# Performance work log

Measured on AMD Instinct MI355X. Metric: run time of the kernel, lower is better.

## Reference

```python
import jax, jax.numpy as jnp
import numpy as np

B, C, H, W, D = 2, 96, 64, 64, 32
NUM_HEADS = 8

def setup_inputs() -> dict:
    key = jax.random.key(0)
    kx, kq, kk, kv, kp = jax.random.split(key, 5)
    x = jax.random.normal(kx, (B, C, H, W, D), dtype=jnp.float32)
    # torch nn.Linear weights: [out_features, in_features]; 1x1x1 conv proj as [C_out, C_in]
    s = 0.02
    Wq = jax.random.normal(kq, (C, C), dtype=jnp.float32) * s
    Wk = jax.random.normal(kk, (C, C), dtype=jnp.float32) * s
    Wv = jax.random.normal(kv, (C, C), dtype=jnp.float32) * s
    Wproj = jax.random.normal(kp, (C, C), dtype=jnp.float32) * s
    return {"x": x, "Wq": Wq, "Wk": Wk, "Wv": Wv, "Wproj": Wproj}

def reference(x, Wq, Wk, Wv, Wproj):
    b, c, h, w, d = x.shape
    n = h * w * d
    nh = NUM_HEADS
    hd = c // nh  # head dim (qk_dim == v_dim == dim here)
    # [B, C, H, W, D] -> [B, N, C]
    xf = jnp.transpose(x.reshape(b, c, n), (0, 2, 1))
    def to_heads(W):
        y = jnp.einsum('bnc,oc->bno', xf, W)  # nn.Linear: x @ W^T
        return jnp.transpose(y.reshape(b, n, nh, hd), (0, 2, 1, 3))  # [B, H, N, hd]
    q = to_heads(Wq)
    k = to_heads(Wk)
    v = to_heads(Wv)
    q = jax.nn.softmax(q, axis=-1)   # over head dim
    k = jax.nn.softmax(k, axis=-2)   # over tokens N
    # linear attention: contract over N first -> tiny [B, H, hd, hd] context
    context = jnp.einsum('bhnd,bhne->bhde', k, v)
    attn = jnp.einsum('bhnd,bhde->bhne', q, context)  # [B, H, N, hd]
    out = jnp.transpose(attn, (0, 2, 1, 3)).reshape(b, n, c)  # [B, N, C]
    out = jnp.transpose(out, (0, 2, 1)).reshape(b, c, h, w, d)
    # 1x1x1 conv projection (bias=False) == channel mixing
    out = jnp.einsum('oc,bchwd->bohwd', Wproj, out)
    return out
```

## Files before the change

kernel.cpp:

```cpp
#include <hip/hip_runtime.h>


typedef _Float16 half_t;
typedef _Float16 half8 __attribute__((ext_vector_type(8)));
typedef float f32x4 __attribute__((ext_vector_type(4)));

#define MFMA16 __builtin_amdgcn_mfma_f32_16x16x32_f16
#define NSH 17
#define NP 16

__device__ __forceinline__ int swz(int row, int colh) {
  return (row * 256 + colh * 2) ^ ((row & 7) << 4);
}

__global__ void wcvt(const float* __restrict__ Wq, const float* __restrict__ Wk,
                     const float* __restrict__ Wv, half_t* __restrict__ WqH,
                     half_t* __restrict__ WkH, half_t* __restrict__ WvH) {
  const int g = blockIdx.x * 256 + threadIdx.x;
  WqH[g] = (half_t)Wq[g];
  WkH[g] = (half_t)Wk[g];
  WvH[g] = (half_t)Wv[g];
}

__global__ __launch_bounds__(256, 3)
void p1(const float* __restrict__ x, const half_t* __restrict__ Wk,
        const half_t* __restrict__ Wv, float* __restrict__ part) {
  __shared__ __align__(16) char smem[49152];

  const int tid  = threadIdx.x;
  const int lane = tid & 63, l15 = lane & 15, quad = lane >> 4, wid = tid >> 6;
  const int b  = blockIdx.x >> 10;
  const int n0 = (blockIdx.x & 1023) << 7;

  float xv[48];
  {
    const float* xb = x + (((size_t)(b * 96 + quad * 8)) << NSH) + n0 + wid * 32 + l15;
#pragma unroll
    for (int ks = 0; ks < 3; ++ks)
#pragma unroll
      for (int j = 0; j < 8; ++j)
#pragma unroll
        for (int ct = 0; ct < 2; ++ct)
          xv[(ks * 8 + j) * 2 + ct] = xb[(((size_t)(ks * 32 + j)) << NSH) + ct * 16];
  }
  half8 bf[3][2];
#pragma unroll
  for (int ks = 0; ks < 3; ++ks)
#pragma unroll
    for (int ct = 0; ct < 2; ++ct)
#pragma unroll
      for (int j = 0; j < 8; ++j)
        bf[ks][ct][j] = (half_t)xv[(ks * 8 + j) * 2 + ct];

  f32x4 acc[6][2];
#pragma unroll
  for (int rt = 0; rt < 6; ++rt)
#pragma unroll
    for (int ct = 0; ct < 2; ++ct) acc[rt][ct] = (f32x4){0.f, 0.f, 0.f, 0.f};
#pragma unroll
  for (int ks = 0; ks < 3; ++ks) {
    half8 af[6];
#pragma unroll
    for (int rt = 0; rt < 6; ++rt)
      af[rt] = *(const half8*)&Wk[(rt * 16 + l15) * 96 + ks * 32 + quad * 8];
#pragma unroll
    for (int rt = 0; rt < 6; ++rt)
#pragma unroll
      for (int ct = 0; ct < 2; ++ct)
        acc[rt][ct] = MFMA16(af[rt], bf[ks][ct], acc[rt][ct], 0, 0, 0);
  }
#pragma unroll
  for (int rt = 0; rt < 6; ++rt)
#pragma unroll
    for (int ct = 0; ct < 2; ++ct)
#pragma unroll
      for (int i = 0; i < 4; ++i) {
        int row = rt * 16 + quad * 4 + i;
        int col = (wid * 2 + ct) * 16 + l15;
        *(half_t*)(smem + swz(row, col)) = (half_t)__expf(acc[rt][ct][i]);
      }

#pragma unroll
  for (int rt = 0; rt < 6; ++rt)
#pragma unroll
    for (int ct = 0; ct < 2; ++ct) acc[rt][ct] = (f32x4){0.f, 0.f, 0.f, 0.f};
#pragma unroll
  for (int ks = 0; ks < 3; ++ks) {
    half8 af[6];
#pragma unroll
    for (int rt = 0; rt < 6; ++rt)
      af[rt] = *(const half8*)&Wv[(rt * 16 + l15) * 96 + ks * 32 + quad * 8];
#pragma unroll
    for (int rt = 0; rt < 6; ++rt)
#pragma unroll
      for (int ct = 0; ct < 2; ++ct)
        acc[rt][ct] = MFMA16(af[rt], bf[ks][ct], acc[rt][ct], 0, 0, 0);
  }
#pragma unroll
  for (int rt = 0; rt < 6; ++rt)
#pragma unroll
    for (int ct = 0; ct < 2; ++ct)
#pragma unroll
      for (int i = 0; i < 4; ++i) {
        int row = rt * 16 + quad * 4 + i;
        int col = (wid * 2 + ct) * 16 + l15;
        *(half_t*)(smem + 24576 + swz(row, col)) = (half_t)acc[rt][ct][i];
      }
  __syncthreads();

  float* dst = part + (size_t)((blockIdx.x & (NP - 1)) * 2 + b) * 1248;
#pragma unroll
  for (int hh = 0; hh < 2; ++hh) {
    const int h = wid * 2 + hh;
    int row = h * 12 + l15; row = row > 95 ? 95 : row;
    f32x4 c = (f32x4){0.f, 0.f, 0.f, 0.f};
#pragma unroll
    for (int ks = 0; ks < 4; ++ks) {
      const int off = swz(row, ks * 32 + quad * 8);
      half8 a  = *(const half8*)(smem + off);
      half8 bv = *(const half8*)(smem + 24576 + off);
      c = MFMA16(a, bv, c, 0, 0, 0);
    }
#pragma unroll
    for (int i = 0; i < 4; ++i) {
      int d = quad * 4 + i, e = l15;
      if (d < 12 && e < 12) atomicAdd(&dst[h * 144 + d * 12 + e], c[i]);
    }
  }
  if (tid < 96) {
    float s = 0.f;
#pragma unroll
    for (int j = 0; j < 16; ++j) {
      half8 v = *(const half8*)(smem + swz(tid, j * 8));
#pragma unroll
      for (int e = 0; e < 8; ++e) s += (float)v[e];
    }
    atomicAdd(&dst[1152 + tid], s);
  }
}

__global__ void kB(const float* __restrict__ part, const float* __restrict__ Wproj,
                   half_t* __restrict__ Mt) {
  const int g = blockIdx.x * 256 + threadIdx.x;
  const int b = g / (96 * 96);
  const int rem = g % (96 * 96);
  const int o = rem / 96;
  const int r = rem % 96;
  const int h = r / 12, d = r % 12;
  float s = 0.f;
#pragma unroll
  for (int p = 0; p < NP; ++p) s += part[(size_t)(p * 2 + b) * 1248 + 1152 + r];
  float acc = 0.f;
#pragma unroll
  for (int e = 0; e < 12; ++e) {
    float ce = 0.f;
#pragma unroll
    for (int p = 0; p < NP; ++p)
      ce += part[(size_t)(p * 2 + b) * 1248 + h * 144 + d * 12 + e];
    acc = fmaf(ce, Wproj[o * 96 + h * 12 + e], acc);
  }
  Mt[(size_t)(b * 96 + o) * 96 + r] = (half_t)(acc / s);
}

__global__ __launch_bounds__(256, 4)
void p3(const float* __restrict__ x, const half_t* __restrict__ Wq,
        const half_t* __restrict__ Mt, float* __restrict__ out) {
  __shared__ __align__(16) char smem[32768];

  const int tid  = threadIdx.x;
  const int lane = tid & 63, l15 = lane & 15, quad = lane >> 4, wid = tid >> 6;
  const int b  = blockIdx.x >> 10;
  const int n0 = (blockIdx.x & 1023) << 7;

  float xv[48];
  {
    const float* xb = x + (((size_t)(b * 96 + quad * 8)) << NSH) + n0 + wid * 32 + l15;
#pragma unroll
    for (int ks = 0; ks < 3; ++ks)
#pragma unroll
      for (int j = 0; j < 8; ++j)
#pragma unroll
        for (int ct = 0; ct < 2; ++ct)
          xv[(ks * 8 + j) * 2 + ct] = xb[(((size_t)(ks * 32 + j)) << NSH) + ct * 16];
  }
  half8 bf[3][2];
#pragma unroll
  for (int ks = 0; ks < 3; ++ks)
#pragma unroll
    for (int ct = 0; ct < 2; ++ct)
#pragma unroll
      for (int j = 0; j < 8; ++j)
        bf[ks][ct][j] = (half_t)xv[(ks * 8 + j) * 2 + ct];

  f32x4 acc[6][2];
#pragma unroll
  for (int rt = 0; rt < 6; ++rt)
#pragma unroll
    for (int ct = 0; ct < 2; ++ct) acc[rt][ct] = (f32x4){0.f, 0.f, 0.f, 0.f};
#pragma unroll
  for (int ks = 0; ks < 3; ++ks) {
    half8 af[6];
#pragma unroll
    for (int rt = 0; rt < 6; ++rt)
      af[rt] = *(const half8*)&Wq[(rt * 16 + l15) * 96 + ks * 32 + quad * 8];
#pragma unroll
    for (int rt = 0; rt < 6; ++rt)
#pragma unroll
      for (int ct = 0; ct < 2; ++ct)
        acc[rt][ct] = MFMA16(af[rt], bf[ks][ct], acc[rt][ct], 0, 0, 0);
  }
#pragma unroll
  for (int rt = 0; rt < 6; ++rt)
#pragma unroll
    for (int ct = 0; ct < 2; ++ct)
#pragma unroll
      for (int i = 0; i < 4; ++i) {
        int row = rt * 16 + quad * 4 + i;
        int col = (wid * 2 + ct) * 16 + l15;
        *(half_t*)(smem + swz(col, row)) = (half_t)acc[rt][ct][i];
      }
  __syncthreads();

  {
    const int n = tid & 127, hg = tid >> 7;
    float q[48];
#pragma unroll
    for (int j = 0; j < 6; ++j) {
      half8 v = *(const half8*)(smem + swz(n, hg * 48 + j * 8));
#pragma unroll
      for (int e = 0; e < 8; ++e) q[j * 8 + e] = (float)v[e];
    }
#pragma unroll
    for (int hh = 0; hh < 4; ++hh) {
      float* ql = q + hh * 12;
      float m = ql[0];
#pragma unroll
      for (int j = 1; j < 12; ++j) m = fmaxf(m, ql[j]);
      float s = 0.f;
#pragma unroll
      for (int j = 0; j < 12; ++j) { ql[j] = __expf(ql[j] - m); s += ql[j]; }
      const float inv = 1.0f / s;
#pragma unroll
      for (int j = 0; j < 12; ++j) ql[j] *= inv;
    }
#pragma unroll
    for (int j = 0; j < 6; ++j) {
      half8 w;
#pragma unroll
      for (int e = 0; e < 8; ++e) w[e] = (half_t)q[j * 8 + e];
      *(half8*)(smem + swz(n, hg * 48 + j * 8)) = w;
    }
  }
  __syncthreads();

#pragma unroll
  for (int rt = 0; rt < 6; ++rt)
#pragma unroll
    for (int ct = 0; ct < 2; ++ct) acc[rt][ct] = (f32x4){0.f, 0.f, 0.f, 0.f};
#pragma unroll
  for (int ks = 0; ks < 3; ++ks) {
    half8 af[6], bq[2];
#pragma unroll
    for (int rt = 0; rt < 6; ++rt)
      af[rt] = *(const half8*)&Mt[(size_t)b * 9216 + (rt * 16 + l15) * 96 + ks * 32 + quad * 8];
#pragma unroll
    for (int ct = 0; ct < 2; ++ct)
      bq[ct] = *(const half8*)(smem + swz((wid * 2 + ct) * 16 + l15, ks * 32 + quad * 8));
#pragma unroll
    for (int rt = 0; rt < 6; ++rt)
#pragma unroll
      for (int ct = 0; ct < 2; ++ct)
        acc[rt][ct] = MFMA16(af[rt], bq[ct], acc[rt][ct], 0, 0, 0);
  }
#pragma unroll
  for (int rt = 0; rt < 6; ++rt)
#pragma unroll
    for (int ct = 0; ct < 2; ++ct)
#pragma unroll
      for (int i = 0; i < 4; ++i) {
        int row = rt * 16 + quad * 4 + i;
        int col = (wid * 2 + ct) * 16 + l15;
        out[(((size_t)(b * 96 + row)) << NSH) + n0 + col] = acc[rt][ct][i];
      }
}

extern "C" void kernel_launch(void* const* d_in, const int* in_sizes, int n_in,
                              void* d_out, int out_size, void* d_ws, size_t ws_size,
                              hipStream_t stream) {
  const float* x     = (const float*)d_in[0];
  const float* Wq    = (const float*)d_in[1];
  const float* Wk    = (const float*)d_in[2];
  const float* Wv    = (const float*)d_in[3];
  const float* Wproj = (const float*)d_in[4];
  float* out = (float*)d_out;
  float* ws  = (float*)d_ws;

  float*  part = ws;
  half_t* Mt   = (half_t*)(ws + NP * 2 * 1248);
  half_t* WqH  = (half_t*)(ws + NP * 2 * 1248 + 9216);
  half_t* WkH  = WqH + 9216;
  half_t* WvH  = WkH + 9216;

  hipMemsetAsync(part, 0, NP * 2 * 1248 * sizeof(float), stream);
  wcvt<<<36, 256, 0, stream>>>(Wq, Wk, Wv, WqH, WkH, WvH);
  p1<<<2048, 256, 0, stream>>>(x, WkH, WvH, part);
  kB<<<72, 256, 0, stream>>>(part, Wproj, Mt);
  p3<<<2048, 256, 0, stream>>>(x, WqH, Mt, out);
}
```

Measured before the change: 246.3 us.

## Use persistent 4-tile blocks with register prefetch and fold context reduction into output kernel

Each block of the K/V-context and output kernels now processes four 128-token tiles, preloading the next tile's x values into registers while computing the current one. The memset is folded into the weight-conversion kernel, and the kB kernel is removed: each output block reduces the partial contexts and builds the projected context matrix in LDS. This cuts launch count and per-block setup. In exchange every output block redundantly recomputes the 96x96 matrix, and occupancy is lower because of larger LDS use and launch bounds of 2.

```diff
diff --git a/kernel.cpp b/kernel.cpp
--- a/kernel.cpp
+++ b/kernel.cpp
@@ -13,28 +13,32 @@
   return (row * 256 + colh * 2) ^ ((row & 7) << 4);
 }
 
-__global__ void wcvt(const float* __restrict__ Wq, const float* __restrict__ Wk,
-                     const float* __restrict__ Wv, half_t* __restrict__ WqH,
-                     half_t* __restrict__ WkH, half_t* __restrict__ WvH) {
+__global__ void k1(const float* __restrict__ Wq, const float* __restrict__ Wk,
+                   const float* __restrict__ Wv, half_t* __restrict__ WqH,
+                   half_t* __restrict__ WkH, half_t* __restrict__ WvH,
+                   float* __restrict__ part) {
   const int g = blockIdx.x * 256 + threadIdx.x;
   WqH[g] = (half_t)Wq[g];
   WkH[g] = (half_t)Wk[g];
   WvH[g] = (half_t)Wv[g];
-}
-
-__global__ __launch_bounds__(256, 3)
-void p1(const float* __restrict__ x, const half_t* __restrict__ Wk,
-        const half_t* __restrict__ Wv, float* __restrict__ part) {
+  for (int i = g; i < NP * 2 * 1248; i += 9216) part[i] = 0.f;
+}
+
+__global__ __launch_bounds__(256, 2)
+void pA(const float* __restrict__ x, const half_t* __restrict__ WkH,
+        const half_t* __restrict__ WvH, float* __restrict__ part) {
   __shared__ __align__(16) char smem[49152];
 
   const int tid  = threadIdx.x;
   const int lane = tid & 63, l15 = lane & 15, quad = lane >> 4, wid = tid >> 6;
-  const int b  = blockIdx.x >> 10;
-  const int n0 = (blockIdx.x & 1023) << 7;
+  const int bid  = blockIdx.x;
+  const int b    = bid >> 8;
+  const float* xbase = x + (((size_t)(b * 96 + quad * 8)) << NSH) + wid * 32 + l15;
+  float* dst = part + (size_t)((bid & (NP - 1)) * 2 + b) * 1248;
 
   float xv[48];
   {
-    const float* xb = x + (((size_t)(b * 96 + quad * 8)) << NSH) + n0 + wid * 32 + l15;
+    const float* xb = xbase + (((bid & 255) * 4 + 0) << 7);
 #pragma unroll
     for (int ks = 0; ks < 3; ++ks)
 #pragma unroll
@@ -43,138 +47,135 @@
         for (int ct = 0; ct < 2; ++ct)
           xv[(ks * 8 + j) * 2 + ct] = xb[(((size_t)(ks * 32 + j)) << NSH) + ct * 16];
   }
-  half8 bf[3][2];
-#pragma unroll
-  for (int ks = 0; ks < 3; ++ks)
-#pragma unroll
-    for (int ct = 0; ct < 2; ++ct)
-#pragma unroll
-      for (int j = 0; j < 8; ++j)
-        bf[ks][ct][j] = (half_t)xv[(ks * 8 + j) * 2 + ct];
-
-  f32x4 acc[6][2];
-#pragma unroll
-  for (int rt = 0; rt < 6; ++rt)
-#pragma unroll
-    for (int ct = 0; ct < 2; ++ct) acc[rt][ct] = (f32x4){0.f, 0.f, 0.f, 0.f};
-#pragma unroll
-  for (int ks = 0; ks < 3; ++ks) {
-    half8 af[6];
-#pragma unroll
-    for (int rt = 0; rt < 6; ++rt)
-      af[rt] = *(const half8*)&Wk[(rt * 16 + l15) * 96 + ks * 32 + quad * 8];
-#pragma unroll
-    for (int rt = 0; rt < 6; ++rt)
-#pragma unroll
-      for (int ct = 0; ct < 2; ++ct)
-        acc[rt][ct] = MFMA16(af[rt], bf[ks][ct], acc[rt][ct], 0, 0, 0);
-  }
-#pragma unroll
-  for (int rt = 0; rt < 6; ++rt)
-#pragma unroll
-    for (int ct = 0; ct < 2; ++ct)
+
+#pragma unroll
+  for (int tt = 0; tt < 4; ++tt) {
+    half8 bf[3][2];
+#pragma unroll
+    for (int ks = 0; ks < 3; ++ks)
+#pragma unroll
+      for (int ct = 0; ct < 2; ++ct)
+#pragma unroll
+        for (int j = 0; j < 8; ++j)
+          bf[ks][ct][j] = (half_t)xv[(ks * 8 + j) * 2 + ct];
+
+    if (tt < 3) {
+      const float* xb = xbase + (((bid & 255) * 4 + tt + 1) << 7);
+#pragma unroll
+      for (int ks = 0; ks < 3; ++ks)
+#pragma unroll
+        for (int j = 0; j < 8; ++j)
+#pragma unroll
+          for (int ct = 0; ct < 2; ++ct)
+            xv[(ks * 8 + j) * 2 + ct] = xb[(((size_t)(ks * 32 + j)) << NSH) + ct * 16];
+    }
+
+    f32x4 acc[6][2];
+#pragma unroll
+    for (int rt = 0; rt < 6; ++rt)
+#pragma unroll
+      for (int ct = 0; ct < 2; ++ct) acc[rt][ct] = (f32x4){0.f, 0.f, 0.f, 0.f};
+#pragma unroll
+    for (int ks = 0; ks < 3; ++ks) {
+      half8 af[6];
+#pragma unroll
+      for (int rt = 0; rt < 6; ++rt)
+        af[rt] = *(const half8*)&WkH[(rt * 16 + l15) * 96 + ks * 32 + quad * 8];
+#pragma unroll
+      for (int rt = 0; rt < 6; ++rt)
+#pragma unroll
+        for (int ct = 0; ct < 2; ++ct)
+          acc[rt][ct] = MFMA16(af[rt], bf[ks][ct], acc[rt][ct], 0, 0, 0);
+    }
+#pragma unroll
+    for (int rt = 0; rt < 6; ++rt)
+#pragma unroll
+      for (int ct = 0; ct < 2; ++ct)
+#pragma unroll
+        for (int i = 0; i < 4; ++i) {
+          int row = rt * 16 + quad * 4 + i;
+          int col = (wid * 2 + ct) * 16 + l15;
+          *(half_t*)(smem + swz(row, col)) = (half_t)__expf(acc[rt][ct][i]);
+        }
+
+#pragma unroll
+    for (int rt = 0; rt < 6; ++rt)
+#pragma unroll
+      for (int ct = 0; ct < 2; ++ct) acc[rt][ct] = (f32x4){0.f, 0.f, 0.f, 0.f};
+#pragma unroll
+    for (int ks = 0; ks < 3; ++ks) {
+      half8 af[6];
+#pragma unroll
+      for (int rt = 0; rt < 6; ++rt)
+        af[rt] = *(const half8*)&WvH[(rt * 16 + l15) * 96 + ks * 32 + quad * 8];
+#pragma unroll
+      for (int rt = 0; rt < 6; ++rt)
+#pragma unroll
+        for (int ct = 0; ct < 2; ++ct)
+          acc[rt][ct] = MFMA16(af[rt], bf[ks][ct], acc[rt][ct], 0, 0, 0);
+    }
+#pragma unroll
+    for (int rt = 0; rt < 6; ++rt)
+#pragma unroll
+      for (int ct = 0; ct < 2; ++ct)
+#pragma unroll
+        for (int i = 0; i < 4; ++i) {
+          int row = rt * 16 + quad * 4 + i;
+          int col = (wid * 2 + ct) * 16 + l15;
+          *(half_t*)(smem + 24576 + swz(row, col)) = (half_t)acc[rt][ct][i];
+        }
+    __syncthreads();
+
+#pragma unroll
+    for (int hh = 0; hh < 2; ++hh) {
+      const int h = wid * 2 + hh;
+      int row = h * 12 + l15; row = row > 95 ? 95 : row;
+      f32x4 c = (f32x4){0.f, 0.f, 0.f, 0.f};
+#pragma unroll
+      for (int ks = 0; ks < 4; ++ks) {
+        const int off = swz(row, ks * 32 + quad * 8);
+        half8 a  = *(const half8*)(smem + off);
+        half8 bv = *(const half8*)(smem + 24576 + off);
+        c = MFMA16(a, bv, c, 0, 0, 0);
+      }
 #pragma unroll
       for (int i = 0; i < 4; ++i) {
-        int row = rt * 16 + quad * 4 + i;
-        int col = (wid * 2 + ct) * 16 + l15;
-        *(half_t*)(smem + swz(row, col)) = (half_t)__expf(acc[rt][ct][i]);
-      }
-
-#pragma unroll
-  for (int rt = 0; rt < 6; ++rt)
-#pragma unroll
-    for (int ct = 0; ct < 2; ++ct) acc[rt][ct] = (f32x4){0.f, 0.f, 0.f, 0.f};
-#pragma unroll
-  for (int ks = 0; ks < 3; ++ks) {
-    half8 af[6];
-#pragma unroll
-    for (int rt = 0; rt < 6; ++rt)
-      af[rt] = *(const half8*)&Wv[(rt * 16 + l15) * 96 + ks * 32 + quad * 8];
-#pragma unroll
-    for (int rt = 0; rt < 6; ++rt)
-#pragma unroll
-      for (int ct = 0; ct < 2; ++ct)
-        acc[rt][ct] = MFMA16(af[rt], bf[ks][ct], acc[rt][ct], 0, 0, 0);
-  }
-#pragma unroll
-  for (int rt = 0; rt < 6; ++rt)
-#pragma unroll
-    for (int ct = 0; ct < 2; ++ct)
-#pragma unroll
-      for (int i = 0; i < 4; ++i) {
-        int row = rt * 16 + quad * 4 + i;
-        int col = (wid * 2 + ct) * 16 + l15;
-        *(half_t*)(smem + 24576 + swz(row, col)) = (half_t)acc[rt][ct][i];
-      }
-  __syncthreads();
-
-  float* dst = part + (size_t)((blockIdx.x & (NP - 1)) * 2 + b) * 1248;
-#pragma unroll
-  for (int hh = 0; hh < 2; ++hh) {
-    const int h = wid * 2 + hh;
-    int row = h * 12 + l15; row = row > 95 ? 95 : row;
-    f32x4 c = (f32x4){0.f, 0.f, 0.f, 0.f};
-#pragma unroll
-    for (int ks = 0; ks < 4; ++ks) {
-      const int off = swz(row, ks * 32 + quad * 8);
-      half8 a  = *(const half8*)(smem + off);
-      half8 bv = *(const half8*)(smem + 24576 + off);
-      c = MFMA16(a, bv, c, 0, 0, 0);
-    }
-#pragma unroll
-    for (int i = 0; i < 4; ++i) {
-      int d = quad * 4 + i, e = l15;
-      if (d < 12 && e < 12) atomicAdd(&dst[h * 144 + d * 12 + e], c[i]);
-    }
-  }
-  if (tid < 96) {
-    float s = 0.f;
-#pragma unroll
-    for (int j = 0; j < 16; ++j) {
-      half8 v = *(const half8*)(smem + swz(tid, j * 8));
-#pragma unroll
-      for (int e = 0; e < 8; ++e) s += (float)v[e];
-    }
-    atomicAdd(&dst[1152 + tid], s);
-  }
-}
-
-__global__ void kB(const float* __restrict__ part, const float* __restrict__ Wproj,
-                   half_t* __restrict__ Mt) {
-  const int g = blockIdx.x * 256 + threadIdx.x;
-  const int b = g / (96 * 96);
-  const int rem = g % (96 * 96);
-  const int o = rem / 96;
-  const int r = rem % 96;
-  const int h = r / 12, d = r % 12;
-  float s = 0.f;
-#pragma unroll
-  for (int p = 0; p < NP; ++p) s += part[(size_t)(p * 2 + b) * 1248 + 1152 + r];
-  float acc = 0.f;
-#pragma unroll
-  for (int e = 0; e < 12; ++e) {
-    float ce = 0.f;
-#pragma unroll
-    for (int p = 0; p < NP; ++p)
-      ce += part[(size_t)(p * 2 + b) * 1248 + h * 144 + d * 12 + e];
-    acc = fmaf(ce, Wproj[o * 96 + h * 12 + e], acc);
-  }
-  Mt[(size_t)(b * 96 + o) * 96 + r] = (half_t)(acc / s);
-}
-
-__global__ __launch_bounds__(256, 4)
-void p3(const float* __restrict__ x, const half_t* __restrict__ Wq,
-        const half_t* __restrict__ Mt, float* __restrict__ out) {
-  __shared__ __align__(16) char smem[32768];
+        int d = quad * 4 + i, e = l15;
+        if (d < 12 && e < 12) atomicAdd(&dst[h * 144 + d * 12 + e], c[i]);
+      }
+    }
+    if (tid < 96) {
+      float s = 0.f;
+#pragma unroll
+      for (int j = 0; j < 16; ++j) {
+        half8 v = *(const half8*)(smem + swz(tid, j * 8));
+#pragma unroll
+        for (int e = 0; e < 8; ++e) s += (float)v[e];
+      }
+      atomicAdd(&dst[1152 + tid], s);
+    }
+    __syncthreads();
+  }
+}
+
+__global__ __launch_bounds__(256, 2)
+void pC(const float* __restrict__ x, const half_t* __restrict__ WqH,
+        const float* __restrict__ Wproj, const float* __restrict__ part,
+        float* __restrict__ out) {
+  __shared__ __align__(16) char smem[53248];
+  half_t* Mt_lds = (half_t*)smem;
+  float*  ctxS   = (float*)(smem + 20480);
+  char*   qs     = smem + 20480;
 
   const int tid  = threadIdx.x;
   const int lane = tid & 63, l15 = lane & 15, quad = lane >> 4, wid = tid >> 6;
-  const int b  = blockIdx.x >> 10;
-  const int n0 = (blockIdx.x & 1023) << 7;
+  const int bid  = blockIdx.x;
+  const int b    = bid >> 8;
+  const float* xbase = x + (((size_t)(b * 96 + quad * 8)) << NSH) + wid * 32 + l15;
 
   float xv[48];
   {
-    const float* xb = x + (((size_t)(b * 96 + quad * 8)) << NSH) + n0 + wid * 32 + l15;
+    const float* xb = xbase + (((bid & 255) * 4 + 0) << 7);
 #pragma unroll
     for (int ks = 0; ks < 3; ++ks)
 #pragma unroll
@@ -183,105 +184,143 @@
         for (int ct = 0; ct < 2; ++ct)
           xv[(ks * 8 + j) * 2 + ct] = xb[(((size_t)(ks * 32 + j)) << NSH) + ct * 16];
   }
-  half8 bf[3][2];
-#pragma unroll
-  for (int ks = 0; ks < 3; ++ks)
-#pragma unroll
-    for (int ct = 0; ct < 2; ++ct)
-#pragma unroll
-      for (int j = 0; j < 8; ++j)
-        bf[ks][ct][j] = (half_t)xv[(ks * 8 + j) * 2 + ct];
-
-  f32x4 acc[6][2];
-#pragma unroll
-  for (int rt = 0; rt < 6; ++rt)
-#pragma unroll
-    for (int ct = 0; ct < 2; ++ct) acc[rt][ct] = (f32x4){0.f, 0.f, 0.f, 0.f};
-#pragma unroll
-  for (int ks = 0; ks < 3; ++ks) {
-    half8 af[6];
-#pragma unroll
-    for (int rt = 0; rt < 6; ++rt)
-      af[rt] = *(const half8*)&Wq[(rt * 16 + l15) * 96 + ks * 32 + quad * 8];
-#pragma unroll
-    for (int rt = 0; rt < 6; ++rt)
-#pragma unroll
-      for (int ct = 0; ct < 2; ++ct)
-        acc[rt][ct] = MFMA16(af[rt], bf[ks][ct], acc[rt][ct], 0, 0, 0);
-  }
-#pragma unroll
-  for (int rt = 0; rt < 6; ++rt)
-#pragma unroll
-    for (int ct = 0; ct < 2; ++ct)
-#pragma unroll
-      for (int i = 0; i < 4; ++i) {
-        int row = rt * 16 + quad * 4 + i;
-        int col = (wid * 2 + ct) * 16 + l15;
-        *(half_t*)(smem + swz(col, row)) = (half_t)acc[rt][ct][i];
-      }
+
+  for (int idx = tid; idx < 1248; idx += 256) {
+    float s = 0.f;
+#pragma unroll
+    for (int p = 0; p < NP; ++p) s += part[(size_t)(p * 2 + b) * 1248 + idx];
+    ctxS[idx] = s;
+  }
   __syncthreads();
-
-  {
-    const int n = tid & 127, hg = tid >> 7;
-    float q[48];
-#pragma unroll
-    for (int j = 0; j < 6; ++j) {
-      half8 v = *(const half8*)(smem + swz(n, hg * 48 + j * 8));
-#pragma unroll
-      for (int e = 0; e < 8; ++e) q[j * 8 + e] = (float)v[e];
-    }
-#pragma unroll
-    for (int hh = 0; hh < 4; ++hh) {
-      float* ql = q + hh * 12;
-      float m = ql[0];
-#pragma unroll
-      for (int j = 1; j < 12; ++j) m = fmaxf(m, ql[j]);
-      float s = 0.f;
-#pragma unroll
-      for (int j = 0; j < 12; ++j) { ql[j] = __expf(ql[j] - m); s += ql[j]; }
-      const float inv = 1.0f / s;
-#pragma unroll
-      for (int j = 0; j < 12; ++j) ql[j] *= inv;
-    }
-#pragma unroll
-    for (int j = 0; j < 6; ++j) {
-      half8 w;
-#pragma unroll
-      for (int e = 0; e < 8; ++e) w[e] = (half_t)q[j * 8 + e];
-      *(half8*)(smem + swz(n, hg * 48 + j * 8)) = w;
-    }
+#pragma unroll
+  for (int i = 0; i < 36; ++i) {
+    int g = i * 256 + tid;
+    int o = g / 96, r = g - o * 96;
+    int h = r / 12, d = r - h * 12;
+    float s = ctxS[1152 + r];
+    float acc = 0.f;
+#pragma unroll
+    for (int e = 0; e < 12; ++e)
+      acc = fmaf(ctxS[h * 144 + d * 12 + e], Wproj[o * 96 + h * 12 + e], acc);
+    Mt_lds[o * 104 + r] = (half_t)(acc / s);
   }
   __syncthreads();
 
 #pragma unroll
-  for (int rt = 0; rt < 6; ++rt)
-#pragma unroll
-    for (int ct = 0; ct < 2; ++ct) acc[rt][ct] = (f32x4){0.f, 0.f, 0.f, 0.f};
-#pragma unroll
-  for (int ks = 0; ks < 3; ++ks) {
-    half8 af[6], bq[2];
-#pragma unroll
-    for (int rt = 0; rt < 6; ++rt)
-      af[rt] = *(const half8*)&Mt[(size_t)b * 9216 + (rt * 16 + l15) * 96 + ks * 32 + quad * 8];
-#pragma unroll
-    for (int ct = 0; ct < 2; ++ct)
-      bq[ct] = *(const half8*)(smem + swz((wid * 2 + ct) * 16 + l15, ks * 32 + quad * 8));
-#pragma unroll
-    for (int rt = 0; rt < 6; ++rt)
-#pragma unroll
-      for (int ct = 0; ct < 2; ++ct)
-        acc[rt][ct] = MFMA16(af[rt], bq[ct], acc[rt][ct], 0, 0, 0);
-  }
-#pragma unroll
-  for (int rt = 0; rt < 6; ++rt)
-#pragma unroll
-    for (int ct = 0; ct < 2; ++ct)
-#pragma unroll
-      for (int i = 0; i < 4; ++i) {
-        int row = rt * 16 + quad * 4 + i;
-        int col = (wid * 2 + ct) * 16 + l15;
-        out[(((size_t)(b * 96 + row)) << NSH) + n0 + col] = acc[rt][ct][i];
-      }
+  for (int tt = 0; tt < 4; ++tt) {
+    half8 bf[3][2];
+#pragma unroll
+    for (int ks = 0; ks < 3; ++ks)
+#pragma unroll
+      for (int ct = 0; ct < 2; ++ct)
+#pragma unroll
+        for (int j = 0; j < 8; ++j)
+          bf[ks][ct][j] = (half_t)xv[(ks * 8 + j) * 2 + ct];
+
+    if (tt < 3) {
+      const float* xb = xbase + (((bid & 255) * 4 + tt + 1) << 7);
+#pragma unroll
+      for (int ks = 0; ks < 3; ++ks)
+#pragma unroll
+        for (int j = 0; j < 8; ++j)
+#pragma unroll
+          for (int ct = 0; ct < 2; ++ct)
+            xv[(ks * 8 + j) * 2 + ct] = xb[(((size_t)(ks * 32 + j)) << NSH) + ct * 16];
+    }
+
+    const int n0 = (((bid & 255) * 4 + tt)) << 7;
+    f32x4 acc[6][2];
+#pragma unroll
+    for (int rt = 0; rt < 6; ++rt)
+#pragma unroll
+      for (int ct = 0; ct < 2; ++ct) acc[rt][ct] = (f32x4){0.f, 0.f, 0.f, 0.f};
+#pragma unroll
+    for (int ks = 0; ks < 3; ++ks) {
+      half8 af[6];
+#pragma unroll
+      for (int rt = 0; rt < 6; ++rt)
+        af[rt] = *(const half8*)&WqH[(rt * 16 + l15) * 96 + ks * 32 + quad * 8];
+#pragma unroll
+      for (int rt = 0; rt < 6; ++rt)
+#pragma unroll
+        for (int ct = 0; ct < 2; ++ct)
+          acc[rt][ct] = MFMA16(af[rt], bf[ks][ct], acc[rt][ct], 0, 0, 0);
+    }
+#pragma unroll
+    for (int rt = 0; rt < 6; ++rt)
+#pragma unroll
+      for (int ct = 0; ct < 2; ++ct)
+#pragma unroll
+        for (int i = 0; i < 4; ++i) {
+          int row = rt * 16 + quad * 4 + i;
+          int col = (wid * 2 + ct) * 16 + l15;
+          *(half_t*)(qs + swz(col, row)) = (half_t)acc[rt][ct][i];
+        }
+    __syncthreads();
+
+    {
+      const int n = tid & 127, hg = tid >> 7;
+      float q[48];
+#pragma unroll
+      for (int j = 0; j < 6; ++j) {
+        half8 v = *(const half8*)(qs + swz(n, hg * 48 + j * 8));
+#pragma unroll
+        for (int e = 0; e < 8; ++e) q[j * 8 + e] = (float)v[e];
+      }
+#pragma unroll
+      for (int hh = 0; hh < 4; ++hh) {
+        float* ql = q + hh * 12;
+        float m = ql[0];
+#pragma unroll
+        for (int j = 1; j < 12; ++j) m = fmaxf(m, ql[j]);
+        float s = 0.f;
+#pragma unroll
+        for (int j = 0; j < 12; ++j) { ql[j] = __expf(ql[j] - m); s += ql[j]; }
+        const float inv = 1.0f / s;
+#pragma unroll
+        for (int j = 0; j < 12; ++j) ql[j] *= inv;
+      }
+#pragma unroll
+      for (int j = 0; j < 6; ++j) {
+        half8 w;
+#pragma unroll
+        for (int e = 0; e < 8; ++e) w[e] = (half_t)q[j * 8 + e];
+        *(half8*)(qs + swz(n, hg * 48 + j * 8)) = w;
+      }
+    }
+    __syncthreads();
+
+#pragma unroll
+    for (int rt = 0; rt < 6; ++rt)
+#pragma unroll
+      for (int ct = 0; ct < 2; ++ct) acc[rt][ct] = (f32x4){0.f, 0.f, 0.f, 0.f};
+#pragma unroll
+    for (int ks = 0; ks < 3; ++ks) {
+      half8 af[6], bq[2];
+#pragma unroll
+      for (int rt = 0; rt < 6; ++rt)
+        af[rt] = *(const half8*)(smem + (rt * 16 + l15) * 208 + (ks * 32 + quad * 8) * 2);
+#pragma unroll
+      for (int ct = 0; ct < 2; ++ct)
+        bq[ct] = *(const half8*)(qs + swz((wid * 2 + ct) * 16 + l15, ks * 32 + quad * 8));
+#pragma unroll
+      for (int rt = 0; rt < 6; ++rt)
+#pragma unroll
+        for (int ct = 0; ct < 2; ++ct)
+          acc[rt][ct] = MFMA16(af[rt], bq[ct], acc[rt][ct], 0, 0, 0);
+    }
+#pragma unroll
+    for (int rt = 0; rt < 6; ++rt)
+#pragma unroll
+      for (int ct = 0; ct < 2; ++ct)
+#pragma unroll
+        for (int i = 0; i < 4; ++i) {
+          int row = rt * 16 + quad * 4 + i;
+          int col = (wid * 2 + ct) * 16 + l15;
+          out[(((size_t)(b * 96 + row)) << NSH) + n0 + col] = acc[rt][ct][i];
+        }
+    __syncthreads();
+  }
 }
 
 extern "C" void kernel_launch(void* const* d_in, const int* in_sizes, int n_in,
@@ -296,14 +335,11 @@
   float* ws  = (float*)d_ws;
 
   float*  part = ws;
-  half_t* Mt   = (half_t*)(ws + NP * 2 * 1248);
-  half_t* WqH  = (half_t*)(ws + NP * 2 * 1248 + 9216);
+  half_t* WqH  = (half_t*)(ws + NP * 2 * 1248);
   half_t* WkH  = WqH + 9216;
   half_t* WvH  = WkH + 9216;
 
-  hipMemsetAsync(part, 0, NP * 2 * 1248 * sizeof(float), stream);
-  wcvt<<<36, 256, 0, stream>>>(Wq, Wk, Wv, WqH, WkH, WvH);
-  p1<<<2048, 256, 0, stream>>>(x, WkH, WvH, part);
-  kB<<<72, 256, 0, stream>>>(part, Wproj, Mt);
-  p3<<<2048, 256, 0, stream>>>(x, WqH, Mt, out);
-}
+  k1<<<36, 256, 0, stream>>>(Wq, Wk, Wv, WqH, WkH, WvH, part);
+  pA<<<512, 256, 0, stream>>>(x, WkH, WvH, part);
+  pC<<<512, 256, 0, stream>>>(x, WqH, Wproj, part, out);
+}
```

After: 271.3 us. 10.2% more time.

## Halve per-block token tile, double partial slots, fold memset into weight kernel

Applied to the files above, without the earlier changes.

Both main kernels now process 64 tokens per block instead of 128, which doubles the grid to 4096 blocks, halves shared memory and registers per block, and raises p1's occupancy bound from 3 to 4. The partial-sum buffer grows from 16 to 32 slots to spread atomic contention over more blocks. The separate memset is folded into the weight-conversion kernel, removing one launch. In exchange, each block reuses its weight fragments over fewer tokens, and twice as many blocks issue atomics.

```diff
diff --git a/kernel.cpp b/kernel.cpp
--- a/kernel.cpp
+++ b/kernel.cpp
@@ -7,118 +7,108 @@
 
 #define MFMA16 __builtin_amdgcn_mfma_f32_16x16x32_f16
 #define NSH 17
-#define NP 16
-
-__device__ __forceinline__ int swz(int row, int colh) {
+#define NP 32
+
+__device__ __forceinline__ int swz64(int row, int colh) {
+  return (row * 128 + colh * 2) ^ ((row & 7) << 4);
+}
+__device__ __forceinline__ int swz128(int row, int colh) {
   return (row * 256 + colh * 2) ^ ((row & 7) << 4);
 }
 
-__global__ void wcvt(const float* __restrict__ Wq, const float* __restrict__ Wk,
-                     const float* __restrict__ Wv, half_t* __restrict__ WqH,
-                     half_t* __restrict__ WkH, half_t* __restrict__ WvH) {
+__global__ void k1(const float* __restrict__ Wq, const float* __restrict__ Wk,
+                   const float* __restrict__ Wv, half_t* __restrict__ WqH,
+                   half_t* __restrict__ WkH, half_t* __restrict__ WvH,
+                   float* __restrict__ part) {
   const int g = blockIdx.x * 256 + threadIdx.x;
   WqH[g] = (half_t)Wq[g];
   WkH[g] = (half_t)Wk[g];
   WvH[g] = (half_t)Wv[g];
-}
-
-__global__ __launch_bounds__(256, 3)
-void p1(const float* __restrict__ x, const half_t* __restrict__ Wk,
-        const half_t* __restrict__ Wv, float* __restrict__ part) {
-  __shared__ __align__(16) char smem[49152];
+  for (int i = g; i < NP * 2 * 1248; i += 9216) part[i] = 0.f;
+}
+
+__global__ __launch_bounds__(256, 4)
+void pA(const float* __restrict__ x, const half_t* __restrict__ WkH,
+        const half_t* __restrict__ WvH, float* __restrict__ part) {
+  __shared__ __align__(16) char smem[24576];
 
   const int tid  = threadIdx.x;
   const int lane = tid & 63, l15 = lane & 15, quad = lane >> 4, wid = tid >> 6;
-  const int b  = blockIdx.x >> 10;
-  const int n0 = (blockIdx.x & 1023) << 7;
-
-  float xv[48];
+  const int bid  = blockIdx.x;
+  const int b    = bid >> 11;
+  const int n0   = (bid & 2047) << 6;
+  float* dst = part + (size_t)((bid & (NP - 1)) * 2 + b) * 1248;
+
+  half8 bf[3];
   {
-    const float* xb = x + (((size_t)(b * 96 + quad * 8)) << NSH) + n0 + wid * 32 + l15;
-#pragma unroll
-    for (int ks = 0; ks < 3; ++ks)
-#pragma unroll
-      for (int j = 0; j < 8; ++j)
-#pragma unroll
-        for (int ct = 0; ct < 2; ++ct)
-          xv[(ks * 8 + j) * 2 + ct] = xb[(((size_t)(ks * 32 + j)) << NSH) + ct * 16];
-  }
-  half8 bf[3][2];
-#pragma unroll
-  for (int ks = 0; ks < 3; ++ks)
-#pragma unroll
-    for (int ct = 0; ct < 2; ++ct)
-#pragma unroll
-      for (int j = 0; j < 8; ++j)
-        bf[ks][ct][j] = (half_t)xv[(ks * 8 + j) * 2 + ct];
-
-  f32x4 acc[6][2];
-#pragma unroll
-  for (int rt = 0; rt < 6; ++rt)
-#pragma unroll
-    for (int ct = 0; ct < 2; ++ct) acc[rt][ct] = (f32x4){0.f, 0.f, 0.f, 0.f};
+    float xv[24];
+    const float* xb = x + (((size_t)(b * 96 + quad * 8)) << NSH) + n0 + wid * 16 + l15;
+#pragma unroll
+    for (int ks = 0; ks < 3; ++ks)
+#pragma unroll
+      for (int j = 0; j < 8; ++j)
+        xv[ks * 8 + j] = xb[(((size_t)(ks * 32 + j)) << NSH)];
+#pragma unroll
+    for (int ks = 0; ks < 3; ++ks)
+#pragma unroll
+      for (int j = 0; j < 8; ++j)
+        bf[ks][j] = (half_t)xv[ks * 8 + j];
+  }
+
+  f32x4 acc[6];
+#pragma unroll
+  for (int rt = 0; rt < 6; ++rt) acc[rt] = (f32x4){0.f, 0.f, 0.f, 0.f};
 #pragma unroll
   for (int ks = 0; ks < 3; ++ks) {
     half8 af[6];
 #pragma unroll
     for (int rt = 0; rt < 6; ++rt)
-      af[rt] = *(const half8*)&Wk[(rt * 16 + l15) * 96 + ks * 32 + quad * 8];
-#pragma unroll
-    for (int rt = 0; rt < 6; ++rt)
-#pragma unroll
-      for (int ct = 0; ct < 2; ++ct)
-        acc[rt][ct] = MFMA16(af[rt], bf[ks][ct], acc[rt][ct], 0, 0, 0);
-  }
-#pragma unroll
-  for (int rt = 0; rt < 6; ++rt)
-#pragma unroll
-    for (int ct = 0; ct < 2; ++ct)
-#pragma unroll
-      for (int i = 0; i < 4; ++i) {
-        int row = rt * 16 + quad * 4 + i;
-        int col = (wid * 2 + ct) * 16 + l15;
-        *(half_t*)(smem + swz(row, col)) = (half_t)__expf(acc[rt][ct][i]);
-      }
-
-#pragma unroll
-  for (int rt = 0; rt < 6; ++rt)
-#pragma unroll
-    for (int ct = 0; ct < 2; ++ct) acc[rt][ct] = (f32x4){0.f, 0.f, 0.f, 0.f};
+      af[rt] = *(const half8*)&WkH[(rt * 16 + l15) * 96 + ks * 32 + quad * 8];
+#pragma unroll
+    for (int rt = 0; rt < 6; ++rt)
+      acc[rt] = MFMA16(af[rt], bf[ks], acc[rt], 0, 0, 0);
+  }
+#pragma unroll
+  for (int rt = 0; rt < 6; ++rt)
+#pragma unroll
+    for (int i = 0; i < 4; ++i) {
+      int row = rt * 16 + quad * 4 + i;
+      int col = wid * 16 + l15;
+      *(half_t*)(smem + swz64(row, col)) = (half_t)__expf(acc[rt][i]);
+    }
+
+#pragma unroll
+  for (int rt = 0; rt < 6; ++rt) acc[rt] = (f32x4){0.f, 0.f, 0.f, 0.f};
 #pragma unroll
   for (int ks = 0; ks < 3; ++ks) {
     half8 af[6];
 #pragma unroll
     for (int rt = 0; rt < 6; ++rt)
-      af[rt] = *(const half8*)&Wv[(rt * 16 + l15) * 96 + ks * 32 + quad * 8];
-#pragma unroll
-    for (int rt = 0; rt < 6; ++rt)
-#pragma unroll
-      for (int ct = 0; ct < 2; ++ct)
-        acc[rt][ct] = MFMA16(af[rt], bf[ks][ct], acc[rt][ct], 0, 0, 0);
-  }
-#pragma unroll
-  for (int rt = 0; rt < 6; ++rt)
-#pragma unroll
-    for (int ct = 0; ct < 2; ++ct)
-#pragma unroll
-      for (int i = 0; i < 4; ++i) {
-        int row = rt * 16 + quad * 4 + i;
-        int col = (wid * 2 + ct) * 16 + l15;
-        *(half_t*)(smem + 24576 + swz(row, col)) = (half_t)acc[rt][ct][i];
-      }
+      af[rt] = *(const half8*)&WvH[(rt * 16 + l15) * 96 + ks * 32 + quad * 8];
+#pragma unroll
+    for (int rt = 0; rt < 6; ++rt)
+      acc[rt] = MFMA16(af[rt], bf[ks], acc[rt], 0, 0, 0);
+  }
+#pragma unroll
+  for (int rt = 0; rt < 6; ++rt)
+#pragma unroll
+    for (int i = 0; i < 4; ++i) {
+      int row = rt * 16 + quad * 4 + i;
+      int col = wid * 16 + l15;
+      *(half_t*)(smem + 12288 + swz64(row, col)) = (half_t)acc[rt][i];
+    }
   __syncthreads();
 
-  float* dst = part + (size_t)((blockIdx.x & (NP - 1)) * 2 + b) * 1248;
 #pragma unroll
   for (int hh = 0; hh < 2; ++hh) {
     const int h = wid * 2 + hh;
     int row = h * 12 + l15; row = row > 95 ? 95 : row;
     f32x4 c = (f32x4){0.f, 0.f, 0.f, 0.f};
 #pragma unroll
-    for (int ks = 0; ks < 4; ++ks) {
-      const int off = swz(row, ks * 32 + quad * 8);
+    for (int ks = 0; ks < 2; ++ks) {
+      const int off = swz64(row, ks * 32 + quad * 8);
       half8 a  = *(const half8*)(smem + off);
-      half8 bv = *(const half8*)(smem + 24576 + off);
+      half8 bv = *(const half8*)(smem + 12288 + off);
       c = MFMA16(a, bv, c, 0, 0, 0);
     }
 #pragma unroll
@@ -130,8 +120,8 @@
   if (tid < 96) {
     float s = 0.f;
 #pragma unroll
-    for (int j = 0; j < 16; ++j) {
-      half8 v = *(const half8*)(smem + swz(tid, j * 8));
+    for (int j = 0; j < 8; ++j) {
+      half8 v = *(const half8*)(smem + swz64(tid, j * 8));
 #pragma unroll
       for (int e = 0; e < 8; ++e) s += (float)v[e];
     }
@@ -163,75 +153,66 @@
 }
 
 __global__ __launch_bounds__(256, 4)
-void p3(const float* __restrict__ x, const half_t* __restrict__ Wq,
+void pC(const float* __restrict__ x, const half_t* __restrict__ WqH,
         const half_t* __restrict__ Mt, float* __restrict__ out) {
-  __shared__ __align__(16) char smem[32768];
+  __shared__ __align__(16) char smem[16384];
 
   const int tid  = threadIdx.x;
   const int lane = tid & 63, l15 = lane & 15, quad = lane >> 4, wid = tid >> 6;
-  const int b  = blockIdx.x >> 10;
-  const int n0 = (blockIdx.x & 1023) << 7;
-
-  float xv[48];
+  const int bid  = blockIdx.x;
+  const int b    = bid >> 11;
+  const int n0   = (bid & 2047) << 6;
+
+  half8 bf[3];
   {
-    const float* xb = x + (((size_t)(b * 96 + quad * 8)) << NSH) + n0 + wid * 32 + l15;
-#pragma unroll
-    for (int ks = 0; ks < 3; ++ks)
-#pragma unroll
-      for (int j = 0; j < 8; ++j)
-#pragma unroll
-        for (int ct = 0; ct < 2; ++ct)
-          xv[(ks * 8 + j) * 2 + ct] = xb[(((size_t)(ks * 32 + j)) << NSH) + ct * 16];
-  }
-  half8 bf[3][2];
-#pragma unroll
-  for (int ks = 0; ks < 3; ++ks)
-#pragma unroll
-    for (int ct = 0; ct < 2; ++ct)
-#pragma unroll
-      for (int j = 0; j < 8; ++j)
-        bf[ks][ct][j] = (half_t)xv[(ks * 8 + j) * 2 + ct];
-
-  f32x4 acc[6][2];
-#pragma unroll
-  for (int rt = 0; rt < 6; ++rt)
-#pragma unroll
-    for (int ct = 0; ct < 2; ++ct) acc[rt][ct] = (f32x4){0.f, 0.f, 0.f, 0.f};
+    float xv[24];
+    const float* xb = x + (((size_t)(b * 96 + quad * 8)) << NSH) + n0 + wid * 16 + l15;
+#pragma unroll
+    for (int ks = 0; ks < 3; ++ks)
+#pragma unroll
+      for (int j = 0; j < 8; ++j)
+        xv[ks * 8 + j] = xb[(((size_t)(ks * 32 + j)) << NSH)];
+#pragma unroll
+    for (int ks = 0; ks < 3; ++ks)
+#pragma unroll
+      for (int j = 0; j < 8; ++j)
+        bf[ks][j] = (half_t)xv[ks * 8 + j];
+  }
+
+  f32x4 acc[6];
+#pragma unroll
+  for (int rt = 0; rt < 6; ++rt) acc[rt] = (f32x4){0.f, 0.f, 0.f, 0.f};
 #pragma unroll
   for (int ks = 0; ks < 3; ++ks) {
     half8 af[6];
 #pragma unroll
     for (int rt = 0; rt < 6; ++rt)
-      af[rt] = *(const half8*)&Wq[(rt * 16 + l15) * 96 + ks * 32 + quad * 8];
-#pragma unroll
-    for (int rt = 0; rt < 6; ++rt)
-#pragma unroll
-      for (int ct = 0; ct < 2; ++ct)
-        acc[rt][ct] = MFMA16(af[rt], bf[ks][ct], acc[rt][ct], 0, 0, 0);
-  }
-#pragma unroll
-  for (int rt = 0; rt < 6; ++rt)
-#pragma unroll
-    for (int ct = 0; ct < 2; ++ct)
-#pragma unroll
-      for (int i = 0; i < 4; ++i) {
-        int row = rt * 16 + quad * 4 + i;
-        int col = (wid * 2 + ct) * 16 + l15;
-        *(half_t*)(smem + swz(col, row)) = (half_t)acc[rt][ct][i];
-      }
+      af[rt] = *(const half8*)&WqH[(rt * 16 + l15) * 96 + ks * 32 + quad * 8];
+#pragma unroll
+    for (int rt = 0; rt < 6; ++rt)
+      acc[rt] = MFMA16(af[rt], bf[ks], acc[rt], 0, 0, 0);
+  }
+#pragma unroll
+  for (int rt = 0; rt < 6; ++rt)
+#pragma unroll
+    for (int i = 0; i < 4; ++i) {
+      int ch  = rt * 16 + quad * 4 + i;
+      int tok = wid * 16 + l15;
+      *(half_t*)(smem + swz128(tok, ch)) = (half_t)acc[rt][i];
+    }
   __syncthreads();
 
   {
-    const int n = tid & 127, hg = tid >> 7;
-    float q[48];
-#pragma unroll
-    for (int j = 0; j < 6; ++j) {
-      half8 v = *(const half8*)(smem + swz(n, hg * 48 + j * 8));
+    const int n = tid & 63, hg = tid >> 6;
+    float q[24];
+#pragma unroll
+    for (int j = 0; j < 3; ++j) {
+      half8 v = *(const half8*)(smem + swz128(n, hg * 24 + j * 8));
 #pragma unroll
       for (int e = 0; e < 8; ++e) q[j * 8 + e] = (float)v[e];
     }
 #pragma unroll
-    for (int hh = 0; hh < 4; ++hh) {
+    for (int hh = 0; hh < 2; ++hh) {
       float* ql = q + hh * 12;
       float m = ql[0];
 #pragma unroll
@@ -244,44 +225,36 @@
       for (int j = 0; j < 12; ++j) ql[j] *= inv;
     }
 #pragma unroll
-    for (int j = 0; j < 6; ++j) {
+    for (int j = 0; j < 3; ++j) {
       half8 w;
 #pragma unroll
       for (int e = 0; e < 8; ++e) w[e] = (half_t)q[j * 8 + e];
-      *(half8*)(smem + swz(n, hg * 48 + j * 8)) = w;
+      *(half8*)(smem + swz128(n, hg * 24 + j * 8)) = w;
     }
   }
   __syncthreads();
 
 #pragma unroll
-  for (int rt = 0; rt < 6; ++rt)
-#pragma unroll
-    for (int ct = 0; ct < 2; ++ct) acc[rt][ct] = (f32x4){0.f, 0.f, 0.f, 0.f};
-#pragma unroll
-  for (int ks = 0; ks < 3; ++ks) {
-    half8 af[6], bq[2];
+  for (int rt = 0; rt < 6; ++rt) acc[rt] = (f32x4){0.f, 0.f, 0.f, 0.f};
+#pragma unroll
+  for (int ks = 0; ks < 3; ++ks) {
+    half8 af[6], bq;
 #pragma unroll
     for (int rt = 0; rt < 6; ++rt)
       af[rt] = *(const half8*)&Mt[(size_t)b * 9216 + (rt * 16 + l15) * 96 + ks * 32 + quad * 8];
-#pragma unroll
-    for (int ct = 0; ct < 2; ++ct)
-      bq[ct] = *(const half8*)(smem + swz((wid * 2 + ct) * 16 + l15, ks * 32 + quad * 8));
-#pragma unroll
-    for (int rt = 0; rt < 6; ++rt)
-#pragma unroll
-      for (int ct = 0; ct < 2; ++ct)
-        acc[rt][ct] = MFMA16(af[rt], bq[ct], acc[rt][ct], 0, 0, 0);
-  }
-#pragma unroll
-  for (int rt = 0; rt < 6; ++rt)
-#pragma unroll
-    for (int ct = 0; ct < 2; ++ct)
-#pragma unroll
-      for (int i = 0; i < 4; ++i) {
-        int row = rt * 16 + quad * 4 + i;
-        int col = (wid * 2 + ct) * 16 + l15;
-        out[(((size_t)(b * 96 + row)) << NSH) + n0 + col] = acc[rt][ct][i];
-      }
+    bq = *(const half8*)(smem + swz128(wid * 16 + l15, ks * 32 + quad * 8));
+#pragma unroll
+    for (int rt = 0; rt < 6; ++rt)
+      acc[rt] = MFMA16(af[rt], bq, acc[rt], 0, 0, 0);
+  }
+#pragma unroll
+  for (int rt = 0; rt < 6; ++rt)
+#pragma unroll
+    for (int i = 0; i < 4; ++i) {
+      int row = rt * 16 + quad * 4 + i;
+      int col = wid * 16 + l15;
+      out[(((size_t)(b * 96 + row)) << NSH) + n0 + col] = acc[rt][i];
+    }
 }
 
 extern "C" void kernel_launch(void* const* d_in, const int* in_sizes, int n_in,
@@ -296,14 +269,13 @@
   float* ws  = (float*)d_ws;
 
   float*  part = ws;
-  half_t* Mt   = (half_t*)(ws + NP * 2 * 1248);
+  half_t* MtH  = (half_t*)(ws + NP * 2 * 1248);
   half_t* WqH  = (half_t*)(ws + NP * 2 * 1248 + 9216);
   half_t* WkH  = WqH + 9216;
   half_t* WvH  = WkH + 9216;
 
-  hipMemsetAsync(part, 0, NP * 2 * 1248 * sizeof(float), stream);
-  wcvt<<<36, 256, 0, stream>>>(Wq, Wk, Wv, WqH, WkH, WvH);
-  p1<<<2048, 256, 0, stream>>>(x, WkH, WvH, part);
-  kB<<<72, 256, 0, stream>>>(part, Wproj, Mt);
-  p3<<<2048, 256, 0, stream>>>(x, WqH, Mt, out);
-}
+  k1<<<36, 256, 0, stream>>>(Wq, Wk, Wv, WqH, WkH, WvH, part);
+  pA<<<4096, 256, 0, stream>>>(x, WkH, WvH, part);
+  kB<<<72, 256, 0, stream>>>(part, Wproj, MtH);
+  pC<<<4096, 256, 0, stream>>>(x, WqH, MtH, out);
+}
```

Result: slower. 284.3 us (+15.4%).
